# Optimization experiments

Measured on AMD Instinct MI355X. Metric: run time of the kernel, lower is better.

The kernel has to match this reference:

```python
import jax, jax.numpy as jnp
import numpy as np

M = 8
EPS = 1e-5


def _bn(x, gamma, beta):
    # x: [T, N, C]; torch BatchNorm1d on [T, C, N] (training mode) normalizes
    # over batch and length dims -> axes (0, 1) here, biased variance.
    mean = jnp.mean(x, axis=(0, 1))
    var = jnp.var(x, axis=(0, 1))
    return (x - mean) * jax.lax.rsqrt(var + EPS) * gamma + beta


def setup_inputs() -> dict:
    key = jax.random.key(0)
    T, N, E = 128, 256, 128
    ks = jax.random.split(key, 16)
    s = 1.0 / np.sqrt(E)
    inp = {
        "node": jax.random.normal(ks[0], (T, N, E), dtype=jnp.float32),
        "Wq": jax.random.uniform(ks[1], (E, E), jnp.float32, -s, s),
        "bq": jax.random.uniform(ks[2], (E,), jnp.float32, -s, s),
        "Wk": jax.random.uniform(ks[3], (E, E), jnp.float32, -s, s),
        "bk": jax.random.uniform(ks[4], (E,), jnp.float32, -s, s),
        "Wv": jax.random.uniform(ks[5], (E, E), jnp.float32, -s, s),
        "bv": jax.random.uniform(ks[6], (E,), jnp.float32, -s, s),
        "Ww": jax.random.uniform(ks[7], (E, E), jnp.float32, -s, s),
        "bw": jax.random.uniform(ks[8], (E,), jnp.float32, -s, s),
        "Wf1": jax.random.uniform(ks[9], (4 * E, E), jnp.float32, -s, s),
        "bf1": jax.random.uniform(ks[10], (4 * E,), jnp.float32, -s, s),
        "Wf2": jax.random.uniform(ks[11], (E, 4 * E), jnp.float32, -0.5 * s, 0.5 * s),
        "bf2": jax.random.uniform(ks[12], (E,), jnp.float32, -0.5 * s, 0.5 * s),
        "g1": jnp.ones((E,), jnp.float32),
        "be1": jnp.zeros((E,), jnp.float32),
        "g2": jnp.ones((E,), jnp.float32),
        "be2": jnp.zeros((E,), jnp.float32),
        "temp_len": T,
    }
    return inp


def reference(node, Wq, bq, Wk, bk, Wv, bv, Ww, bw, Wf1, bf1, Wf2, bf2,
              g1, be1, g2, be2, temp_len):
    T, N, E = node.shape
    D = E // M          # head dim = 16
    dk = E / M          # softmax scale denominator (embedding_size / M)

    q = (node @ Wq.T + bq).reshape(T, N, M, D)
    k = (node @ Wk.T + bk).reshape(T, N, M, D)
    v = (node @ Wv.T + bv).reshape(T, N, M, D)

    # scores[t,n,j,m] = sum_d q[t,n,m,d]*k[t,j,m,d] / sqrt(dk)
    scores = jnp.einsum('tnmd,tjmd->tnjm', q, k) / jnp.sqrt(jnp.float32(dk))
    attn = jax.nn.softmax(scores, axis=2)  # softmax over key dim (dim=2)

    # out[t,n,m,d] = sum_j attn[t,n,j,m] * v[t,j,m,d]
    out = jnp.einsum('tnjm,tjmd->tnmd', attn, v).reshape(T, N, E)

    x = out @ Ww.T + bw + node
    x = _bn(x, g1, be1)

    x1 = jax.nn.relu(x @ Wf1.T + bf1) @ Wf2.T + bf2
    x = x + x1
    x = _bn(x, g2, be2)
    return x
```

## Files before the change

### kernel.cpp

```cpp
#include <hip/hip_runtime.h>
#include <stdint.h>

typedef unsigned int  uint32;
typedef unsigned short u16;
typedef __attribute__((ext_vector_type(8))) short short8;
typedef __attribute__((ext_vector_type(4))) float f32x4;
typedef __attribute__((ext_vector_type(4))) _Float16 half4;

__device__ __forceinline__ float bits2f(uint32 u){ union{uint32 u; float f;} c; c.u=u; return c.f; }
__device__ __forceinline__ uint32 f2bits(float f){ union{uint32 u; float f;} c; c.f=f; return c.u; }
__device__ __forceinline__ u16 f2b(float f){ uint32 u=f2bits(f); return (u16)((u + 0x7FFFu + ((u>>16)&1u))>>16); }
__device__ __forceinline__ float b2f(u16 h){ return bits2f(((uint32)h)<<16); }
__device__ __forceinline__ u16 f2h(float f){ _Float16 h=(_Float16)f; union{u16 u; _Float16 h;} c; c.h=h; return c.u; }
__device__ __forceinline__ float4 ld4f(const float* p){ return *(const float4*)p; }
#define BLO(u) bits2f((u)<<16)
#define BHI(u) bits2f((u)&0xFFFF0000u)

#define QKS 24

__device__ __forceinline__ void load_ab(const float* __restrict__ gacc,
                                        const float* __restrict__ gam,
                                        const float* __restrict__ bet,
                                        float* sA, float* sB, int t)
{
  if (t < 128) {
    const float mean = gacc[t] * (1.f/32768.f);
    const float var  = gacc[128 + t] * (1.f/32768.f) - mean * mean;
    const float rstd = rsqrtf(var + 1e-5f);
    const float Ac = gam[t] * rstd;
    sA[t] = Ac;
    sB[t] = bet[t] - mean * Ac;
  }
  __syncthreads();
}

template<int OMODE, int RES, bool RELU, bool AF32, bool WF32, bool BNA, bool STATS, int JT>
__device__ __forceinline__ void gemm_tile(
    u16* As, u16* Ws, const float* sA, const float* sB, float* pS, float* pQ,
    const void* Ain, const void* W, const float* bias, const void* res,
    float* gacc_out, void* out, int row0, int col0, int K, int Nout,
    float oscale, int t)
{
  constexpr int WROWS = JT * 32;
  const int L = t & 63, w = t >> 6;
  const int wrow = (w >> 1) * 64, wcol = (w & 1) * (JT * 16);
  const int lm = L & 15, lg = L >> 4;

  f32x4 acc[4][JT];
#pragma unroll
  for (int i = 0; i < 4; ++i)
#pragma unroll
    for (int j = 0; j < JT; ++j) acc[i][j] = (f32x4){0.f,0.f,0.f,0.f};

  const int srow = t >> 1, skc = (t & 1) * 32;
  const u16*   Ab = (const u16*)Ain + (size_t)(row0 + srow) * K + skc;
  const float* Af = (const float*)Ain + (size_t)(row0 + srow) * K + skc;
  u16* Asp = As + srow * 72 + skc;
  constexpr int TPR = 256 / WROWS;
  const int wsrow = t / TPR, wskc = (t % TPR) * (64 / TPR);
  const u16*   Wp  = (const u16*)W + (size_t)(col0 + wsrow) * K + wskc;
  const float* Wpf = (const float*)W + (size_t)(col0 + wsrow) * K + wskc;
  u16* Wsp = Ws + wsrow * 72 + wskc;
  constexpr int NW = (64 / TPR) / 8;

  for (int k0 = 0; k0 < K; k0 += 64) {
    short8 ga[4], gw[NW];
    if constexpr (AF32) {
#pragma unroll
      for (int i = 0; i < 4; ++i) {
        const float4 fa = ld4f(Af + k0 + i*8);
        const float4 fb = ld4f(Af + k0 + i*8 + 4);
        short8 s;
        s[0]=(short)f2b(fa.x); s[1]=(short)f2b(fa.y); s[2]=(short)f2b(fa.z); s[3]=(short)f2b(fa.w);
        s[4]=(short)f2b(fb.x); s[5]=(short)f2b(fb.y); s[6]=(short)f2b(fb.z); s[7]=(short)f2b(fb.w);
        ga[i] = s;
      }
    } else if constexpr (BNA) {
#pragma unroll
      for (int i = 0; i < 4; ++i) {
        const int c = skc + k0 + i*8;
        const short8 x8 = *(const short8*)(Ab + k0 + i*8);
        const float4 A0 = *(const float4*)&sA[c], A1 = *(const float4*)&sA[c+4];
        const float4 B0 = *(const float4*)&sB[c], B1 = *(const float4*)&sB[c+4];
        short8 s;
        s[0]=(short)f2b(b2f((u16)x8[0])*A0.x+B0.x); s[1]=(short)f2b(b2f((u16)x8[1])*A0.y+B0.y);
        s[2]=(short)f2b(b2f((u16)x8[2])*A0.z+B0.z); s[3]=(short)f2b(b2f((u16)x8[3])*A0.w+B0.w);
        s[4]=(short)f2b(b2f((u16)x8[4])*A1.x+B1.x); s[5]=(short)f2b(b2f((u16)x8[5])*A1.y+B1.y);
        s[6]=(short)f2b(b2f((u16)x8[6])*A1.z+B1.z); s[7]=(short)f2b(b2f((u16)x8[7])*A1.w+B1.w);
        ga[i] = s;
      }
    } else {
#pragma unroll
      for (int i = 0; i < 4; ++i) ga[i] = *(const short8*)(Ab + k0 + i*8);
    }
    if constexpr (WF32) {
#pragma unroll
      for (int i = 0; i < NW; ++i) {
        const float4 fa = ld4f(Wpf + k0 + i*8);
        const float4 fb = ld4f(Wpf + k0 + i*8 + 4);
        short8 s;
        s[0]=(short)f2b(fa.x); s[1]=(short)f2b(fa.y); s[2]=(short)f2b(fa.z); s[3]=(short)f2b(fa.w);
        s[4]=(short)f2b(fb.x); s[5]=(short)f2b(fb.y); s[6]=(short)f2b(fb.z); s[7]=(short)f2b(fb.w);
        gw[i] = s;
      }
    } else {
#pragma unroll
      for (int i = 0; i < NW; ++i) gw[i] = *(const short8*)(Wp + k0 + i*8);
    }
    __syncthreads();
#pragma unroll
    for (int i = 0; i < 4; ++i) *(short8*)(Asp + i*8) = ga[i];
#pragma unroll
    for (int i = 0; i < NW; ++i) *(short8*)(Wsp + i*8) = gw[i];
    __syncthreads();
#pragma unroll
    for (int ks = 0; ks < 64; ks += 32) {
      short8 af[4], wf[JT];
#pragma unroll
      for (int i = 0; i < 4; ++i)
        af[i] = *(const short8*)(As + (wrow + i*16 + lm) * 72 + ks + lg*8);
#pragma unroll
      for (int j = 0; j < JT; ++j)
        wf[j] = *(const short8*)(Ws + (wcol + j*16 + lm) * 72 + ks + lg*8);
#pragma unroll
      for (int i = 0; i < 4; ++i)
#pragma unroll
        for (int j = 0; j < JT; ++j)
          acc[i][j] = __builtin_amdgcn_mfma_f32_16x16x32_bf16(af[i], wf[j], acc[i][j], 0, 0, 0);
    }
  }

  float bj[JT];
#pragma unroll
  for (int j = 0; j < JT; ++j) bj[j] = bias[col0 + wcol + j*16 + lm];

  float stS[JT], stQ[JT];
#pragma unroll
  for (int j = 0; j < JT; ++j) { stS[j] = 0.f; stQ[j] = 0.f; }

#pragma unroll
  for (int i = 0; i < 4; ++i) {
    const int rowb = row0 + wrow + i*16 + lg*4;
#pragma unroll
    for (int j = 0; j < JT; ++j) {
      const int col = col0 + wcol + j*16 + lm;
      float ra = 0.f, rb = 0.f;
      if constexpr (RES == 3) { ra = sA[col & 127]; rb = sB[col & 127]; }
      if constexpr (OMODE == 3) {
        const int tt = rowb >> 8, n0 = rowb & 255;
        const int mh = col >> 4, d = col & 15;
        uint2 o;
        o.x = (uint32)f2h(acc[i][j][0] + bj[j]) | ((uint32)f2h(acc[i][j][1] + bj[j]) << 16);
        o.y = (uint32)f2h(acc[i][j][2] + bj[j]) | ((uint32)f2h(acc[i][j][3] + bj[j]) << 16);
        *(uint2*)((u16*)out + (((size_t)tt*8 + mh)*16 + d)*256 + n0) = o;
      } else {
#pragma unroll
        for (int r = 0; r < 4; ++r) {
          const int row = rowb + r;
          float v = acc[i][j][r] + bj[j];
          if constexpr (RES == 1) v += ((const float*)res)[(size_t)row*128 + col];
          if constexpr (RES == 3) v += b2f(((const u16*)res)[(size_t)row*128 + col]) * ra + rb;
          if constexpr (RELU) v = fmaxf(v, 0.f);
          if constexpr (STATS) { stS[j] += v; stQ[j] += v*v; }
          if constexpr (OMODE == 2) {
            const int tt = row >> 8, n = row & 255, mh = col >> 4, d = col & 15;
            ((u16*)out)[(((size_t)tt*8 + mh)*256 + n)*16 + d] = f2h(v * oscale);
          } else {
            ((u16*)out)[(size_t)row * Nout + col] = f2b(v);
          }
        }
      }
    }
  }

  if constexpr (STATS) {
    __syncthreads();
    if (t < 128) { pS[t] = 0.f; pQ[t] = 0.f; }
    __syncthreads();
#pragma unroll
    for (int j = 0; j < JT; ++j) {
      const int col = col0 + wcol + j*16 + lm;
      atomicAdd(&pS[col], stS[j]);
      atomicAdd(&pQ[col], stQ[j]);
    }
    __syncthreads();
    if (t < 128) {
      atomicAdd(&gacc_out[t],       pS[t]);
      atomicAdd(&gacc_out[128 + t], pQ[t]);
    }
  }
}

__global__ __launch_bounds__(256)
void qkv_k(const float* __restrict__ node,
           const float* __restrict__ Wq, const float* __restrict__ bq,
           const float* __restrict__ Wk, const float* __restrict__ bk,
           const float* __restrict__ Wv, const float* __restrict__ bv,
           const float* __restrict__ Ww, const float* __restrict__ Wf1,
           const float* __restrict__ Wf2,
           u16* __restrict__ qb, u16* __restrict__ kb, u16* __restrict__ vb,
           u16* __restrict__ wb, float* __restrict__ accbuf)
{
  const int bid = blockIdx.x, t = threadIdx.x;
  if (bid < 768) {
    __shared__ u16 As[128*72];
    __shared__ u16 Ws[128*72];
    __shared__ __align__(16) float sA[128], sB[128];
    __shared__ float pS[128], pQ[128];
    const int x = bid & 255, y = bid >> 8;
    const float QSCALE = 0.36067376022224085f;
    if (y == 0)
      gemm_tile<2,0,false,true,true,false,false,4>(As,Ws,sA,sB,pS,pQ, node, Wq, bq,
          nullptr, nullptr, qb, x*128, 0, 128, 128, QSCALE, t);
    else if (y == 1)
      gemm_tile<2,0,false,true,true,false,false,4>(As,Ws,sA,sB,pS,pQ, node, Wk, bk,
          nullptr, nullptr, kb, x*128, 0, 128, 128, 1.f, t);
    else
      gemm_tile<3,0,false,true,true,false,false,4>(As,Ws,sA,sB,pS,pQ, node, Wv, bv,
          nullptr, nullptr, vb, x*128, 0, 128, 128, 1.f, t);
  } else if (bid < 912) {
    const int i = (bid - 768) * 256 + t;
    const float4* src; u16* dst;
    if      (i <  4096) { src = (const float4*)Ww  + i;         dst = wb +  49152 + (size_t)i*4; }
    else if (i < 20480) { src = (const float4*)Wf1 + (i-4096);  dst = wb +  65536 + (size_t)(i-4096)*4; }
    else                { src = (const float4*)Wf2 + (i-20480); dst = wb + 131072 + (size_t)(i-20480)*4; }
    float4 v = *src;
    uint2 o;
    o.x = (uint32)f2b(v.x) | ((uint32)f2b(v.y) << 16);
    o.y = (uint32)f2b(v.z) | ((uint32)f2b(v.w) << 16);
    *(uint2*)dst = o;
  } else {
    accbuf[t] = 0.f;
    accbuf[256 + t] = 0.f;
  }
}

__global__ __launch_bounds__(256)
void oproj_k(const u16* __restrict__ ab, const u16* __restrict__ wwb,
             const float* __restrict__ bw, const float* __restrict__ node,
             float* __restrict__ accbuf, u16* __restrict__ xb)
{
  __shared__ u16 As[128*72];
  __shared__ u16 Ws[128*72];
  __shared__ __align__(16) float sA[128], sB[128];
  __shared__ float pS[128], pQ[128];
  gemm_tile<0,1,false,false,false,false,true,4>(As,Ws,sA,sB,pS,pQ, ab, wwb, bw,
      node, accbuf, xb, blockIdx.x*128, 0, 128, 128, 1.f, threadIdx.x);
}

__global__ __launch_bounds__(256)
void ffn1_k(const u16* __restrict__ xb, const u16* __restrict__ wf1b,
            const float* __restrict__ bf1, const float* __restrict__ accbuf,
            const float* __restrict__ g1, const float* __restrict__ be1,
            u16* __restrict__ hb)
{
  __shared__ u16 As[128*72];
  __shared__ u16 Ws[128*72];
  __shared__ __align__(16) float sA[128], sB[128];
  __shared__ float pS[128], pQ[128];
  load_ab(accbuf, g1, be1, sA, sB, threadIdx.x);
  gemm_tile<0,0,true,false,false,true,false,4>(As,Ws,sA,sB,pS,pQ, xb, wf1b, bf1,
      nullptr, nullptr, hb, blockIdx.x*128, blockIdx.y*128, 128, 512, 1.f, threadIdx.x);
}

__global__ __launch_bounds__(256)
void ffn2_k(const u16* __restrict__ hb, const u16* __restrict__ wf2b,
            const float* __restrict__ bf2, const u16* __restrict__ xb,
            const float* __restrict__ accbuf, const float* __restrict__ g1,
            const float* __restrict__ be1, float* __restrict__ acc2,
            u16* __restrict__ x2b)
{
  __shared__ u16 As[128*72];
  __shared__ u16 Ws[64*72];
  __shared__ __align__(16) float sA[128], sB[128];
  __shared__ float pS[128], pQ[128];
  load_ab(accbuf, g1, be1, sA, sB, threadIdx.x);
  gemm_tile<0,3,false,false,false,false,true,2>(As,Ws,sA,sB,pS,pQ, hb, wf2b, bf2,
      xb, acc2, x2b, blockIdx.x*128, blockIdx.y*64, 512, 128, 1.f, threadIdx.x);
}

__global__ __launch_bounds__(256)
void attn_k(const u16* __restrict__ q, const u16* __restrict__ k,
            const u16* __restrict__ v, u16* __restrict__ ab)
{
  __shared__ __align__(16) u16 Qs[256*QKS];
  __shared__ __align__(16) u16 Ks[256*QKS];
  __shared__ __align__(16) u16 Vt[16*264];
  const int tm = blockIdx.x, tt = tm >> 3, m = tm & 7;
  const int t = threadIdx.x;

  const uint4* qg = (const uint4*)(q + (size_t)tm*4096);
  const uint4* kg = (const uint4*)(k + (size_t)tm*4096);
  const uint4* vg = (const uint4*)(v + (size_t)tm*4096);
#pragma unroll
  for (int p = t; p < 512; p += 256) {
    const uint4 a = qg[p], b = kg[p], c = vg[p];
    const int row = p >> 1, h = (p & 1) * 8;
    *(uint4*)(Qs + row*QKS + h) = a;
    *(uint4*)(Ks + row*QKS + h) = b;
    *(uint4*)(Vt + (p >> 5)*264 + (p & 31)*8) = c;
  }
  __syncthreads();

  const int w = t >> 6, L = t & 63, lm = L & 15, quad = L >> 4;

  half4 vf[16];
#pragma unroll
  for (int jt = 0; jt < 16; ++jt)
    vf[jt] = *(const half4*)(Vt + lm*264 + jt*16 + quad*4);

  for (int nt = 0; nt < 4; ++nt) {
    const half4 bq = *(const half4*)(Qs + ((w*4 + nt)*16 + lm)*QKS + quad*4);
    f32x4 s[16];
#pragma unroll
    for (int jt = 0; jt < 16; ++jt) {
      const half4 af = *(const half4*)(Ks + (jt*16 + lm)*QKS + quad*4);
      s[jt] = __builtin_amdgcn_mfma_f32_16x16x16f16(af, bq, (f32x4){0.f,0.f,0.f,0.f}, 0, 0, 0);
    }
    float mx = s[0][0];
#pragma unroll
    for (int jt = 0; jt < 16; ++jt)
#pragma unroll
      for (int r = 0; r < 4; ++r) mx = fmaxf(mx, s[jt][r]);
    mx = fmaxf(mx, __shfl_xor(mx, 16));
    mx = fmaxf(mx, __shfl_xor(mx, 32));
    float ls = 0.f;
#pragma unroll
    for (int jt = 0; jt < 16; ++jt)
#pragma unroll
      for (int r = 0; r < 4; ++r) { const float p = exp2f(s[jt][r] - mx); s[jt][r] = p; ls += p; }
    ls += __shfl_xor(ls, 16);
    ls += __shfl_xor(ls, 32);

    f32x4 oacc = {0.f,0.f,0.f,0.f};
#pragma unroll
    for (int jt = 0; jt < 16; ++jt) {
      half4 pf;
      pf[0] = (_Float16)s[jt][0]; pf[1] = (_Float16)s[jt][1];
      pf[2] = (_Float16)s[jt][2]; pf[3] = (_Float16)s[jt][3];
      oacc = __builtin_amdgcn_mfma_f32_16x16x16f16(pf, vf[jt], oacc, 0, 0, 0);
    }
    const int q0 = w*64 + nt*16 + quad*4;
#pragma unroll
    for (int r = 0; r < 4; ++r) {
      const float lr = __shfl(ls, quad*4 + r);
      ab[((size_t)tt*256 + q0 + r)*128 + m*16 + lm] = f2b(oacc[r] / lr);
    }
  }
}

__global__ __launch_bounds__(256)
void bn_final(const uint32* __restrict__ x2, const float* __restrict__ gacc,
              const float* __restrict__ gam, const float* __restrict__ bet,
              float* __restrict__ out)
{
  __shared__ float sA[128], sB[128];
  const int t = threadIdx.x;
  load_ab(gacc, gam, bet, sA, sB, t);
#pragma unroll 4
  for (int kk = 0; kk < 16; ++kk) {
    const size_t idx = (size_t)blockIdx.x * 4096 + kk * 256 + t;
    const uint32 u = x2[idx];
    const int c = (int)((idx & 63) * 2);
    float2 o;
    o.x = BLO(u) * sA[c]   + sB[c];
    o.y = BHI(u) * sA[c+1] + sB[c+1];
    ((float2*)out)[idx] = o;
  }
}

extern "C" void kernel_launch(void* const* d_in, const int* in_sizes, int n_in,
                              void* d_out, int out_size, void* d_ws, size_t ws_size,
                              hipStream_t stream)
{
  (void)in_sizes; (void)n_in; (void)out_size; (void)ws_size;
  const float* node = (const float*)d_in[0];
  const float* Wq  = (const float*)d_in[1];  const float* bq  = (const float*)d_in[2];
  const float* Wk  = (const float*)d_in[3];  const float* bk  = (const float*)d_in[4];
  const float* Wv  = (const float*)d_in[5];  const float* bv  = (const float*)d_in[6];
  const float* Ww  = (const float*)d_in[7];  const float* bw  = (const float*)d_in[8];
  const float* Wf1 = (const float*)d_in[9];  const float* bf1 = (const float*)d_in[10];
  const float* Wf2 = (const float*)d_in[11]; const float* bf2 = (const float*)d_in[12];
  const float* g1  = (const float*)d_in[13]; const float* be1 = (const float*)d_in[14];
  const float* g2  = (const float*)d_in[15]; const float* be2 = (const float*)d_in[16];
  float* out = (float*)d_out;
  char* ws = (char*)d_ws;

  u16* wb  = (u16*)(ws + 0);
  u16* qb  = (u16*)(ws + 524288);
  u16* kb  = (u16*)(ws + 8912896);
  u16* vb  = (u16*)(ws + 17301504);
  u16* ab  = (u16*)(ws + 25690112);
  u16* xb  = (u16*)(ws + 34078720);
  u16* x2b = (u16*)(ws + 42467328);
  float* accbuf = (float*)(ws + 50855936);
  u16* hb  = qb;

  u16* wwb = wb + 49152;  u16* wf1b = wb + 65536; u16* wf2b = wb + 131072;

  dim3 blk(256);

  qkv_k<<<dim3(913), blk, 0, stream>>>(node, Wq,bq, Wk,bk, Wv,bv, Ww, Wf1, Wf2,
                                       qb, kb, vb, wb, accbuf);
  attn_k<<<dim3(1024), blk, 0, stream>>>(qb, kb, vb, ab);
  oproj_k<<<dim3(256), blk, 0, stream>>>(ab, wwb, bw, node, accbuf, xb);
  ffn1_k<<<dim3(256,4), blk, 0, stream>>>(xb, wf1b, bf1, accbuf, g1, be1, hb);
  ffn2_k<<<dim3(256,2), blk, 0, stream>>>(hb, wf2b, bf2, xb, accbuf, g1, be1,
                                          accbuf + 256, x2b);
  bn_final<<<dim3(512), blk, 0, stream>>>((const uint32*)x2b, accbuf + 256, g2, be2, out);
}
```

Measured before the change: 205.7 us.

## Load GEMM tiles directly into LDS in MFMA fragment layout

The GEMM tile loader is rewritten so that bf16 operands move straight from global memory into shared memory with global_load_lds, in a layout that already matches the MFMA fragments. This removes the register staging step and the padded-row indexing. All weights, including Wq/Wk/Wv, are now converted to bf16 in a separate small kernel ahead of a 2D-grid QKV kernel, so the QKV GEMM no longer converts fp32 weights itself. The output projection is also split across two column blocks to double its grid. The costs are one extra kernel launch and reliance on direct-to-LDS loads. The new unpadded layout also changes how shared-memory reads map to banks.

```diff
diff --git a/kernel.cpp b/kernel.cpp
--- a/kernel.cpp
+++ b/kernel.cpp
@@ -18,6 +18,11 @@
 
 #define QKS 24
 
+__device__ __forceinline__ void gload16(const u16* g, u16* l) {
+  __builtin_amdgcn_global_load_lds((const __attribute__((address_space(1))) void*)g,
+                                   (__attribute__((address_space(3))) void*)l, 16, 0, 0);
+}
+
 __device__ __forceinline__ void load_ab(const float* __restrict__ gacc,
                                         const float* __restrict__ gam,
                                         const float* __restrict__ bet,
@@ -34,17 +39,17 @@
   __syncthreads();
 }
 
-template<int OMODE, int RES, bool RELU, bool AF32, bool WF32, bool BNA, bool STATS, int JT>
+template<int OMODE, int RES, bool RELU, bool AF32, bool BNA, bool STATS, int JT>
 __device__ __forceinline__ void gemm_tile(
     u16* As, u16* Ws, const float* sA, const float* sB, float* pS, float* pQ,
-    const void* Ain, const void* W, const float* bias, const void* res,
+    const void* Ain, const u16* W, const float* bias, const void* res,
     float* gacc_out, void* out, int row0, int col0, int K, int Nout,
     float oscale, int t)
 {
-  constexpr int WROWS = JT * 32;
-  const int L = t & 63, w = t >> 6;
-  const int wrow = (w >> 1) * 64, wcol = (w & 1) * (JT * 16);
+  constexpr int WPAN = JT * 4;
+  const int L = t & 63, wv = t >> 6;
   const int lm = L & 15, lg = L >> 4;
+  const int wrow = (wv >> 1) * 64, wcol = (wv & 1) * (JT * 16);
 
   f32x4 acc[4][JT];
 #pragma unroll
@@ -52,34 +57,25 @@
 #pragma unroll
     for (int j = 0; j < JT; ++j) acc[i][j] = (f32x4){0.f,0.f,0.f,0.f};
 
-  const int srow = t >> 1, skc = (t & 1) * 32;
-  const u16*   Ab = (const u16*)Ain + (size_t)(row0 + srow) * K + skc;
-  const float* Af = (const float*)Ain + (size_t)(row0 + srow) * K + skc;
-  u16* Asp = As + srow * 72 + skc;
-  constexpr int TPR = 256 / WROWS;
-  const int wsrow = t / TPR, wskc = (t % TPR) * (64 / TPR);
-  const u16*   Wp  = (const u16*)W + (size_t)(col0 + wsrow) * K + wskc;
-  const float* Wpf = (const float*)W + (size_t)(col0 + wsrow) * K + wskc;
-  u16* Wsp = Ws + wsrow * 72 + wskc;
-  constexpr int NW = (64 / TPR) / 8;
-
   for (int k0 = 0; k0 < K; k0 += 64) {
-    short8 ga[4], gw[NW];
+    short8 ga[4];
     if constexpr (AF32) {
 #pragma unroll
-      for (int i = 0; i < 4; ++i) {
-        const float4 fa = ld4f(Af + k0 + i*8);
-        const float4 fb = ld4f(Af + k0 + i*8 + 4);
+      for (int pp = 0; pp < 4; ++pp) {
+        const int p = wv*4 + pp, rp = p >> 1, kp = p & 1;
+        const float* g = (const float*)Ain + (size_t)(row0 + rp*16 + lm)*K + k0 + kp*32 + lg*8;
+        const float4 fa = ld4f(g), fb = ld4f(g + 4);
         short8 s;
         s[0]=(short)f2b(fa.x); s[1]=(short)f2b(fa.y); s[2]=(short)f2b(fa.z); s[3]=(short)f2b(fa.w);
         s[4]=(short)f2b(fb.x); s[5]=(short)f2b(fb.y); s[6]=(short)f2b(fb.z); s[7]=(short)f2b(fb.w);
-        ga[i] = s;
+        ga[pp] = s;
       }
     } else if constexpr (BNA) {
 #pragma unroll
-      for (int i = 0; i < 4; ++i) {
-        const int c = skc + k0 + i*8;
-        const short8 x8 = *(const short8*)(Ab + k0 + i*8);
+      for (int pp = 0; pp < 4; ++pp) {
+        const int p = wv*4 + pp, rp = p >> 1, kp = p & 1;
+        const int c = k0 + kp*32 + lg*8;
+        const short8 x8 = *(const short8*)((const u16*)Ain + (size_t)(row0 + rp*16 + lm)*K + c);
         const float4 A0 = *(const float4*)&sA[c], A1 = *(const float4*)&sA[c+4];
         const float4 B0 = *(const float4*)&sB[c], B1 = *(const float4*)&sB[c+4];
         short8 s;
@@ -87,41 +83,38 @@
         s[2]=(short)f2b(b2f((u16)x8[2])*A0.z+B0.z); s[3]=(short)f2b(b2f((u16)x8[3])*A0.w+B0.w);
         s[4]=(short)f2b(b2f((u16)x8[4])*A1.x+B1.x); s[5]=(short)f2b(b2f((u16)x8[5])*A1.y+B1.y);
         s[6]=(short)f2b(b2f((u16)x8[6])*A1.z+B1.z); s[7]=(short)f2b(b2f((u16)x8[7])*A1.w+B1.w);
-        ga[i] = s;
+        ga[pp] = s;
       }
+    }
+    __syncthreads();
+    if constexpr (AF32 || BNA) {
+#pragma unroll
+      for (int pp = 0; pp < 4; ++pp)
+        *(short8*)(As + (wv*4 + pp)*512 + L*8) = ga[pp];
     } else {
 #pragma unroll
-      for (int i = 0; i < 4; ++i) ga[i] = *(const short8*)(Ab + k0 + i*8);
-    }
-    if constexpr (WF32) {
-#pragma unroll
-      for (int i = 0; i < NW; ++i) {
-        const float4 fa = ld4f(Wpf + k0 + i*8);
-        const float4 fb = ld4f(Wpf + k0 + i*8 + 4);
-        short8 s;
-        s[0]=(short)f2b(fa.x); s[1]=(short)f2b(fa.y); s[2]=(short)f2b(fa.z); s[3]=(short)f2b(fa.w);
-        s[4]=(short)f2b(fb.x); s[5]=(short)f2b(fb.y); s[6]=(short)f2b(fb.z); s[7]=(short)f2b(fb.w);
-        gw[i] = s;
+      for (int pp = 0; pp < 4; ++pp) {
+        const int p = wv*4 + pp, rp = p >> 1, kp = p & 1;
+        gload16((const u16*)Ain + (size_t)(row0 + rp*16 + lm)*K + k0 + kp*32 + lg*8,
+                As + p*512);
       }
-    } else {
-#pragma unroll
-      for (int i = 0; i < NW; ++i) gw[i] = *(const short8*)(Wp + k0 + i*8);
+    }
+#pragma unroll
+    for (int pp = 0; pp < WPAN/4; ++pp) {
+      const int p = wv*(WPAN/4) + pp, rp = p >> 1, kp = p & 1;
+      gload16(W + (size_t)(col0 + rp*16 + lm)*K + k0 + kp*32 + lg*8, Ws + p*512);
     }
     __syncthreads();
 #pragma unroll
-    for (int i = 0; i < 4; ++i) *(short8*)(Asp + i*8) = ga[i];
-#pragma unroll
-    for (int i = 0; i < NW; ++i) *(short8*)(Wsp + i*8) = gw[i];
-    __syncthreads();
-#pragma unroll
     for (int ks = 0; ks < 64; ks += 32) {
+      const int kp = ks >> 5;
       short8 af[4], wf[JT];
 #pragma unroll
       for (int i = 0; i < 4; ++i)
-        af[i] = *(const short8*)(As + (wrow + i*16 + lm) * 72 + ks + lg*8);
+        af[i] = *(const short8*)(As + ((((wrow >> 4) + i)*2 + kp) << 9) + L*8);
 #pragma unroll
       for (int j = 0; j < JT; ++j)
-        wf[j] = *(const short8*)(Ws + (wcol + j*16 + lm) * 72 + ks + lg*8);
+        wf[j] = *(const short8*)(Ws + ((((wcol >> 4) + j)*2 + kp) << 9) + L*8);
 #pragma unroll
       for (int i = 0; i < 4; ++i)
 #pragma unroll
@@ -192,47 +185,49 @@
 }
 
 __global__ __launch_bounds__(256)
-void qkv_k(const float* __restrict__ node,
-           const float* __restrict__ Wq, const float* __restrict__ bq,
-           const float* __restrict__ Wk, const float* __restrict__ bk,
-           const float* __restrict__ Wv, const float* __restrict__ bv,
-           const float* __restrict__ Ww, const float* __restrict__ Wf1,
-           const float* __restrict__ Wf2,
-           u16* __restrict__ qb, u16* __restrict__ kb, u16* __restrict__ vb,
+void cvt_w(const float4* __restrict__ wq, const float4* __restrict__ wk,
+           const float4* __restrict__ wv, const float4* __restrict__ ww,
+           const float4* __restrict__ wf1, const float4* __restrict__ wf2,
            u16* __restrict__ wb, float* __restrict__ accbuf)
 {
-  const int bid = blockIdx.x, t = threadIdx.x;
-  if (bid < 768) {
-    __shared__ u16 As[128*72];
-    __shared__ u16 Ws[128*72];
-    __shared__ __align__(16) float sA[128], sB[128];
-    __shared__ float pS[128], pQ[128];
-    const int x = bid & 255, y = bid >> 8;
-    const float QSCALE = 0.36067376022224085f;
-    if (y == 0)
-      gemm_tile<2,0,false,true,true,false,false,4>(As,Ws,sA,sB,pS,pQ, node, Wq, bq,
-          nullptr, nullptr, qb, x*128, 0, 128, 128, QSCALE, t);
-    else if (y == 1)
-      gemm_tile<2,0,false,true,true,false,false,4>(As,Ws,sA,sB,pS,pQ, node, Wk, bk,
-          nullptr, nullptr, kb, x*128, 0, 128, 128, 1.f, t);
-    else
-      gemm_tile<3,0,false,true,true,false,false,4>(As,Ws,sA,sB,pS,pQ, node, Wv, bv,
-          nullptr, nullptr, vb, x*128, 0, 128, 128, 1.f, t);
-  } else if (bid < 912) {
-    const int i = (bid - 768) * 256 + t;
-    const float4* src; u16* dst;
-    if      (i <  4096) { src = (const float4*)Ww  + i;         dst = wb +  49152 + (size_t)i*4; }
-    else if (i < 20480) { src = (const float4*)Wf1 + (i-4096);  dst = wb +  65536 + (size_t)(i-4096)*4; }
-    else                { src = (const float4*)Wf2 + (i-20480); dst = wb + 131072 + (size_t)(i-20480)*4; }
-    float4 v = *src;
-    uint2 o;
-    o.x = (uint32)f2b(v.x) | ((uint32)f2b(v.y) << 16);
-    o.y = (uint32)f2b(v.z) | ((uint32)f2b(v.w) << 16);
-    *(uint2*)dst = o;
-  } else {
-    accbuf[t] = 0.f;
-    accbuf[256 + t] = 0.f;
-  }
+  const int t = threadIdx.x;
+  if (blockIdx.x == 192) { accbuf[t] = 0.f; accbuf[256 + t] = 0.f; return; }
+  const int i = blockIdx.x * 256 + t;
+  const float4* src;
+  if      (i <  4096) src = wq  + i;
+  else if (i <  8192) src = wk  + (i-4096);
+  else if (i < 12288) src = wv  + (i-8192);
+  else if (i < 16384) src = ww  + (i-12288);
+  else if (i < 32768) src = wf1 + (i-16384);
+  else                src = wf2 + (i-32768);
+  float4 v = *src;
+  uint2 o;
+  o.x = (uint32)f2b(v.x) | ((uint32)f2b(v.y) << 16);
+  o.y = (uint32)f2b(v.z) | ((uint32)f2b(v.w) << 16);
+  *(uint2*)(wb + (size_t)i*4) = o;
+}
+
+__global__ __launch_bounds__(256)
+void qkv_k(const float* __restrict__ node, const u16* __restrict__ wb,
+           const float* __restrict__ bq, const float* __restrict__ bk,
+           const float* __restrict__ bv,
+           u16* __restrict__ qb, u16* __restrict__ kb, u16* __restrict__ vb)
+{
+  __shared__ __align__(16) u16 As[8192];
+  __shared__ __align__(16) u16 Ws[8192];
+  __shared__ __align__(16) float sA[128], sB[128];
+  __shared__ float pS[128], pQ[128];
+  const int x = blockIdx.x, y = blockIdx.y, t = threadIdx.x;
+  const float QSCALE = 0.36067376022224085f;
+  if (y == 0)
+    gemm_tile<2,0,false,true,false,false,4>(As,Ws,sA,sB,pS,pQ, node, wb, bq,
+        nullptr, nullptr, qb, x*128, 0, 128, 128, QSCALE, t);
+  else if (y == 1)
+    gemm_tile<2,0,false,true,false,false,4>(As,Ws,sA,sB,pS,pQ, node, wb + 16384, bk,
+        nullptr, nullptr, kb, x*128, 0, 128, 128, 1.f, t);
+  else
+    gemm_tile<3,0,false,true,false,false,4>(As,Ws,sA,sB,pS,pQ, node, wb + 32768, bv,
+        nullptr, nullptr, vb, x*128, 0, 128, 128, 1.f, t);
 }
 
 __global__ __launch_bounds__(256)
@@ -240,12 +235,12 @@
              const float* __restrict__ bw, const float* __restrict__ node,
              float* __restrict__ accbuf, u16* __restrict__ xb)
 {
-  __shared__ u16 As[128*72];
-  __shared__ u16 Ws[128*72];
+  __shared__ __align__(16) u16 As[8192];
+  __shared__ __align__(16) u16 Ws[4096];
   __shared__ __align__(16) float sA[128], sB[128];
   __shared__ float pS[128], pQ[128];
-  gemm_tile<0,1,false,false,false,false,true,4>(As,Ws,sA,sB,pS,pQ, ab, wwb, bw,
-      node, accbuf, xb, blockIdx.x*128, 0, 128, 128, 1.f, threadIdx.x);
+  gemm_tile<0,1,false,false,false,true,2>(As,Ws,sA,sB,pS,pQ, ab, wwb, bw,
+      node, accbuf, xb, blockIdx.x*128, blockIdx.y*64, 128, 128, 1.f, threadIdx.x);
 }
 
 __global__ __launch_bounds__(256)
@@ -254,12 +249,12 @@
             const float* __restrict__ g1, const float* __restrict__ be1,
             u16* __restrict__ hb)
 {
-  __shared__ u16 As[128*72];
-  __shared__ u16 Ws[128*72];
+  __shared__ __align__(16) u16 As[8192];
+  __shared__ __align__(16) u16 Ws[8192];
   __shared__ __align__(16) float sA[128], sB[128];
   __shared__ float pS[128], pQ[128];
   load_ab(accbuf, g1, be1, sA, sB, threadIdx.x);
-  gemm_tile<0,0,true,false,false,true,false,4>(As,Ws,sA,sB,pS,pQ, xb, wf1b, bf1,
+  gemm_tile<0,0,true,false,true,false,4>(As,Ws,sA,sB,pS,pQ, xb, wf1b, bf1,
       nullptr, nullptr, hb, blockIdx.x*128, blockIdx.y*128, 128, 512, 1.f, threadIdx.x);
 }
 
@@ -270,12 +265,12 @@
             const float* __restrict__ be1, float* __restrict__ acc2,
             u16* __restrict__ x2b)
 {
-  __shared__ u16 As[128*72];
-  __shared__ u16 Ws[64*72];
+  __shared__ __align__(16) u16 As[8192];
+  __shared__ __align__(16) u16 Ws[4096];
   __shared__ __align__(16) float sA[128], sB[128];
   __shared__ float pS[128], pQ[128];
   load_ab(accbuf, g1, be1, sA, sB, threadIdx.x);
-  gemm_tile<0,3,false,false,false,false,true,2>(As,Ws,sA,sB,pS,pQ, hb, wf2b, bf2,
+  gemm_tile<0,3,false,false,false,true,2>(As,Ws,sA,sB,pS,pQ, hb, wf2b, bf2,
       xb, acc2, x2b, blockIdx.x*128, blockIdx.y*64, 512, 128, 1.f, threadIdx.x);
 }
 
@@ -400,10 +395,12 @@
 
   dim3 blk(256);
 
-  qkv_k<<<dim3(913), blk, 0, stream>>>(node, Wq,bq, Wk,bk, Wv,bv, Ww, Wf1, Wf2,
-                                       qb, kb, vb, wb, accbuf);
+  cvt_w<<<dim3(193), blk, 0, stream>>>((const float4*)Wq, (const float4*)Wk,
+      (const float4*)Wv, (const float4*)Ww, (const float4*)Wf1, (const float4*)Wf2,
+      wb, accbuf);
+  qkv_k<<<dim3(256,3), blk, 0, stream>>>(node, wb, bq, bk, bv, qb, kb, vb);
   attn_k<<<dim3(1024), blk, 0, stream>>>(qb, kb, vb, ab);
-  oproj_k<<<dim3(256), blk, 0, stream>>>(ab, wwb, bw, node, accbuf, xb);
+  oproj_k<<<dim3(256,2), blk, 0, stream>>>(ab, wwb, bw, node, accbuf, xb);
   ffn1_k<<<dim3(256,4), blk, 0, stream>>>(xb, wf1b, bf1, accbuf, g1, be1, hb);
   ffn2_k<<<dim3(256,2), blk, 0, stream>>>(hb, wf2b, bf2, xb, accbuf, g1, be1,
                                           accbuf + 256, x2b);
```

Measured after the change: 214.2 us. 4.1% more time.

## Parameterize GEMM K-tile, use single-stage K for K=128, prefetch in FFN2

Applied to the files above, without the earlier changes.

The shared GEMM tile gains a compile-time K-chunk size and an optional register prefetch. The K=128 GEMMs (QKV, output projection, FFN1) now load the whole K dimension in one stage, which removes a pair of barriers per tile at the cost of more LDS. FFN2 prefetches the next K chunk into registers while the MFMAs run on the current one. The output projection is split into two 64-column tiles per row block, doubling its grid to 512 blocks for better CU occupancy, at the cost of reloading the A tile twice.

```diff
diff --git a/kernel.cpp b/kernel.cpp
--- a/kernel.cpp
+++ b/kernel.cpp
@@ -34,7 +34,8 @@
   __syncthreads();
 }
 
-template<int OMODE, int RES, bool RELU, bool AF32, bool WF32, bool BNA, bool STATS, int JT>
+template<int OMODE, int RES, bool RELU, bool AF32, bool WF32, bool BNA, bool STATS,
+         int JT, int BK, bool PREF>
 __device__ __forceinline__ void gemm_tile(
     u16* As, u16* Ws, const float* sA, const float* sB, float* pS, float* pQ,
     const void* Ain, const void* W, const float* bias, const void* res,
@@ -42,9 +43,13 @@
     float oscale, int t)
 {
   constexpr int WROWS = JT * 32;
-  const int L = t & 63, w = t >> 6;
-  const int wrow = (w >> 1) * 64, wcol = (w & 1) * (JT * 16);
+  constexpr int S   = BK + 8;
+  constexpr int TPR = 256 / WROWS;
+  constexpr int NA  = BK / 16;
+  constexpr int NW  = (BK / TPR) / 8;
+  const int L = t & 63, wv = t >> 6;
   const int lm = L & 15, lg = L >> 4;
+  const int wrow = (wv >> 1) * 64, wcol = (wv & 1) * (JT * 16);
 
   f32x4 acc[4][JT];
 #pragma unroll
@@ -52,22 +57,19 @@
 #pragma unroll
     for (int j = 0; j < JT; ++j) acc[i][j] = (f32x4){0.f,0.f,0.f,0.f};
 
-  const int srow = t >> 1, skc = (t & 1) * 32;
+  const int srow = t >> 1, skc = (t & 1) * (BK / 2);
   const u16*   Ab = (const u16*)Ain + (size_t)(row0 + srow) * K + skc;
   const float* Af = (const float*)Ain + (size_t)(row0 + srow) * K + skc;
-  u16* Asp = As + srow * 72 + skc;
-  constexpr int TPR = 256 / WROWS;
-  const int wsrow = t / TPR, wskc = (t % TPR) * (64 / TPR);
+  u16* Asp = As + srow * S + skc;
+  const int wsrow = t / TPR, wskc = (t % TPR) * (BK / TPR);
   const u16*   Wp  = (const u16*)W + (size_t)(col0 + wsrow) * K + wskc;
   const float* Wpf = (const float*)W + (size_t)(col0 + wsrow) * K + wskc;
-  u16* Wsp = Ws + wsrow * 72 + wskc;
-  constexpr int NW = (64 / TPR) / 8;
-
-  for (int k0 = 0; k0 < K; k0 += 64) {
-    short8 ga[4], gw[NW];
+  u16* Wsp = Ws + wsrow * S + wskc;
+
+  auto loadA = [&](int k0, short8* ga) {
     if constexpr (AF32) {
 #pragma unroll
-      for (int i = 0; i < 4; ++i) {
+      for (int i = 0; i < NA; ++i) {
         const float4 fa = ld4f(Af + k0 + i*8);
         const float4 fb = ld4f(Af + k0 + i*8 + 4);
         short8 s;
@@ -77,7 +79,7 @@
       }
     } else if constexpr (BNA) {
 #pragma unroll
-      for (int i = 0; i < 4; ++i) {
+      for (int i = 0; i < NA; ++i) {
         const int c = skc + k0 + i*8;
         const short8 x8 = *(const short8*)(Ab + k0 + i*8);
         const float4 A0 = *(const float4*)&sA[c], A1 = *(const float4*)&sA[c+4];
@@ -91,8 +93,10 @@
       }
     } else {
 #pragma unroll
-      for (int i = 0; i < 4; ++i) ga[i] = *(const short8*)(Ab + k0 + i*8);
-    }
+      for (int i = 0; i < NA; ++i) ga[i] = *(const short8*)(Ab + k0 + i*8);
+    }
+  };
+  auto loadW = [&](int k0, short8* gw) {
     if constexpr (WF32) {
 #pragma unroll
       for (int i = 0; i < NW; ++i) {
@@ -107,26 +111,56 @@
 #pragma unroll
       for (int i = 0; i < NW; ++i) gw[i] = *(const short8*)(Wp + k0 + i*8);
     }
-    __syncthreads();
-#pragma unroll
-    for (int i = 0; i < 4; ++i) *(short8*)(Asp + i*8) = ga[i];
-#pragma unroll
-    for (int i = 0; i < NW; ++i) *(short8*)(Wsp + i*8) = gw[i];
-    __syncthreads();
-#pragma unroll
-    for (int ks = 0; ks < 64; ks += 32) {
+  };
+  auto mfma_chunk = [&]() {
+#pragma unroll
+    for (int ks = 0; ks < BK; ks += 32) {
       short8 af[4], wf[JT];
 #pragma unroll
       for (int i = 0; i < 4; ++i)
-        af[i] = *(const short8*)(As + (wrow + i*16 + lm) * 72 + ks + lg*8);
+        af[i] = *(const short8*)(As + (wrow + i*16 + lm) * S + ks + lg*8);
 #pragma unroll
       for (int j = 0; j < JT; ++j)
-        wf[j] = *(const short8*)(Ws + (wcol + j*16 + lm) * 72 + ks + lg*8);
+        wf[j] = *(const short8*)(Ws + (wcol + j*16 + lm) * S + ks + lg*8);
 #pragma unroll
       for (int i = 0; i < 4; ++i)
 #pragma unroll
         for (int j = 0; j < JT; ++j)
           acc[i][j] = __builtin_amdgcn_mfma_f32_16x16x32_bf16(af[i], wf[j], acc[i][j], 0, 0, 0);
+    }
+  };
+
+  if constexpr (PREF) {
+    short8 ga[NA], gw[NW], ga2[NA], gw2[NW];
+    loadA(0, ga); loadW(0, gw);
+    for (int k0 = 0; k0 < K; k0 += BK) {
+      __syncthreads();
+#pragma unroll
+      for (int i = 0; i < NA; ++i) *(short8*)(Asp + i*8) = ga[i];
+#pragma unroll
+      for (int i = 0; i < NW; ++i) *(short8*)(Wsp + i*8) = gw[i];
+      __syncthreads();
+      const int kn = k0 + BK;
+      if (kn < K) { loadA(kn, ga2); loadW(kn, gw2); }
+      mfma_chunk();
+      if (kn < K) {
+#pragma unroll
+        for (int i = 0; i < NA; ++i) ga[i] = ga2[i];
+#pragma unroll
+        for (int i = 0; i < NW; ++i) gw[i] = gw2[i];
+      }
+    }
+  } else {
+    for (int k0 = 0; k0 < K; k0 += BK) {
+      short8 ga[NA], gw[NW];
+      loadA(k0, ga); loadW(k0, gw);
+      __syncthreads();
+#pragma unroll
+      for (int i = 0; i < NA; ++i) *(short8*)(Asp + i*8) = ga[i];
+#pragma unroll
+      for (int i = 0; i < NW; ++i) *(short8*)(Wsp + i*8) = gw[i];
+      __syncthreads();
+      mfma_chunk();
     }
   }
 
@@ -203,21 +237,21 @@
 {
   const int bid = blockIdx.x, t = threadIdx.x;
   if (bid < 768) {
-    __shared__ u16 As[128*72];
-    __shared__ u16 Ws[128*72];
+    __shared__ __align__(16) u16 As[128*136];
+    __shared__ __align__(16) u16 Ws[128*136];
     __shared__ __align__(16) float sA[128], sB[128];
     __shared__ float pS[128], pQ[128];
     const int x = bid & 255, y = bid >> 8;
     const float QSCALE = 0.36067376022224085f;
     if (y == 0)
-      gemm_tile<2,0,false,true,true,false,false,4>(As,Ws,sA,sB,pS,pQ, node, Wq, bq,
-          nullptr, nullptr, qb, x*128, 0, 128, 128, QSCALE, t);
+      gemm_tile<2,0,false,true,true,false,false,4,128,false>(As,Ws,sA,sB,pS,pQ,
+          node, Wq, bq, nullptr, nullptr, qb, x*128, 0, 128, 128, QSCALE, t);
     else if (y == 1)
-      gemm_tile<2,0,false,true,true,false,false,4>(As,Ws,sA,sB,pS,pQ, node, Wk, bk,
-          nullptr, nullptr, kb, x*128, 0, 128, 128, 1.f, t);
+      gemm_tile<2,0,false,true,true,false,false,4,128,false>(As,Ws,sA,sB,pS,pQ,
+          node, Wk, bk, nullptr, nullptr, kb, x*128, 0, 128, 128, 1.f, t);
     else
-      gemm_tile<3,0,false,true,true,false,false,4>(As,Ws,sA,sB,pS,pQ, node, Wv, bv,
-          nullptr, nullptr, vb, x*128, 0, 128, 128, 1.f, t);
+      gemm_tile<3,0,false,true,true,false,false,4,128,false>(As,Ws,sA,sB,pS,pQ,
+          node, Wv, bv, nullptr, nullptr, vb, x*128, 0, 128, 128, 1.f, t);
   } else if (bid < 912) {
     const int i = (bid - 768) * 256 + t;
     const float4* src; u16* dst;
@@ -240,12 +274,12 @@
              const float* __restrict__ bw, const float* __restrict__ node,
              float* __restrict__ accbuf, u16* __restrict__ xb)
 {
-  __shared__ u16 As[128*72];
-  __shared__ u16 Ws[128*72];
+  __shared__ __align__(16) u16 As[128*136];
+  __shared__ __align__(16) u16 Ws[64*136];
   __shared__ __align__(16) float sA[128], sB[128];
   __shared__ float pS[128], pQ[128];
-  gemm_tile<0,1,false,false,false,false,true,4>(As,Ws,sA,sB,pS,pQ, ab, wwb, bw,
-      node, accbuf, xb, blockIdx.x*128, 0, 128, 128, 1.f, threadIdx.x);
+  gemm_tile<0,1,false,false,false,false,true,2,128,false>(As,Ws,sA,sB,pS,pQ,
+      ab, wwb, bw, node, accbuf, xb, blockIdx.x*128, blockIdx.y*64, 128, 128, 1.f, threadIdx.x);
 }
 
 __global__ __launch_bounds__(256)
@@ -254,13 +288,13 @@
             const float* __restrict__ g1, const float* __restrict__ be1,
             u16* __restrict__ hb)
 {
-  __shared__ u16 As[128*72];
-  __shared__ u16 Ws[128*72];
+  __shared__ __align__(16) u16 As[128*136];
+  __shared__ __align__(16) u16 Ws[128*136];
   __shared__ __align__(16) float sA[128], sB[128];
   __shared__ float pS[128], pQ[128];
   load_ab(accbuf, g1, be1, sA, sB, threadIdx.x);
-  gemm_tile<0,0,true,false,false,true,false,4>(As,Ws,sA,sB,pS,pQ, xb, wf1b, bf1,
-      nullptr, nullptr, hb, blockIdx.x*128, blockIdx.y*128, 128, 512, 1.f, threadIdx.x);
+  gemm_tile<0,0,true,false,false,true,false,4,128,false>(As,Ws,sA,sB,pS,pQ,
+      xb, wf1b, bf1, nullptr, nullptr, hb, blockIdx.x*128, blockIdx.y*128, 128, 512, 1.f, threadIdx.x);
 }
 
 __global__ __launch_bounds__(256)
@@ -270,13 +304,13 @@
             const float* __restrict__ be1, float* __restrict__ acc2,
             u16* __restrict__ x2b)
 {
-  __shared__ u16 As[128*72];
-  __shared__ u16 Ws[64*72];
+  __shared__ __align__(16) u16 As[128*72];
+  __shared__ __align__(16) u16 Ws[64*72];
   __shared__ __align__(16) float sA[128], sB[128];
   __shared__ float pS[128], pQ[128];
   load_ab(accbuf, g1, be1, sA, sB, threadIdx.x);
-  gemm_tile<0,3,false,false,false,false,true,2>(As,Ws,sA,sB,pS,pQ, hb, wf2b, bf2,
-      xb, acc2, x2b, blockIdx.x*128, blockIdx.y*64, 512, 128, 1.f, threadIdx.x);
+  gemm_tile<0,3,false,false,false,false,true,2,64,true>(As,Ws,sA,sB,pS,pQ,
+      hb, wf2b, bf2, xb, acc2, x2b, blockIdx.x*128, blockIdx.y*64, 512, 128, 1.f, threadIdx.x);
 }
 
 __global__ __launch_bounds__(256)
@@ -403,7 +437,7 @@
   qkv_k<<<dim3(913), blk, 0, stream>>>(node, Wq,bq, Wk,bk, Wv,bv, Ww, Wf1, Wf2,
                                        qb, kb, vb, wb, accbuf);
   attn_k<<<dim3(1024), blk, 0, stream>>>(qb, kb, vb, ab);
-  oproj_k<<<dim3(256), blk, 0, stream>>>(ab, wwb, bw, node, accbuf, xb);
+  oproj_k<<<dim3(256,2), blk, 0, stream>>>(ab, wwb, bw, node, accbuf, xb);
   ffn1_k<<<dim3(256,4), blk, 0, stream>>>(xb, wf1b, bf1, accbuf, g1, be1, hb);
   ffn2_k<<<dim3(256,2), blk, 0, stream>>>(hb, wf2b, bf2, xb, accbuf, g1, be1,
                                           accbuf + 256, x2b);
```

New measurement: 218.2 us. 6.1% more time.
